# Kernel optimization log

Measured on AMD Instinct MI355X. Metric: run time of the kernel, lower is better.

## Reference

```python
import jax, jax.numpy as jnp
import numpy as np

B, NF, NB, E = 32768, 64, 33, 64  # batch, num_features, boundaries per feature, embedding size


def setup_inputs() -> dict:
    key = jax.random.key(0)
    kx, kb, kw = jax.random.split(key, 3)
    X = jax.random.normal(kx, (B, NF), dtype=jnp.float32)
    # strictly increasing per-feature boundaries: cumsum of positive steps
    steps = jax.random.uniform(kb, (NF, NB), dtype=jnp.float32, minval=0.05, maxval=0.2)
    bounds = jnp.cumsum(steps, axis=1) - 2.0  # roughly centered around the data range
    W = jax.random.normal(kw, (NF, NB - 1, E), dtype=jnp.float32) / np.sqrt(NB - 1).astype(np.float32)
    b = jnp.zeros((NF, E), dtype=jnp.float32)
    return {"X": X, "bounds": bounds, "W": W, "b": b}


def reference(X, bounds, W, b):
    # Piecewise-linear bin encoding, vectorized over all features at once.
    lo = bounds[:, :-1]            # [NF, NB-1]
    hi = bounds[:, 1:]             # [NF, NB-1]
    scale = hi - lo                # [NF, NB-1]
    x = X[:, :, None]              # [B, NF, 1]
    enc = (jax.nn.relu(x - lo[None]) - jax.nn.relu(x - hi[None])) / scale  # [B, NF, NB-1]
    # Per-feature Linear + ReLU (block-diagonal / grouped GEMM), then concat over features
    out = jax.nn.relu(jnp.einsum('bfi,fie->bfe', enc, W) + b[None])       # [B, NF, E]
    return out.reshape(X.shape[0], -1)                                     # [B, NF*E]
```

## Files before the change

### kernel.cpp

```cpp
#include <hip/hip_runtime.h>

#define B_TOT 32768
#define NF    64
#define NB    33
#define NSEG  32
#define E     64
#define BPB   256

__global__ __launch_bounds__(256) void pwl_kernel(
    const float* __restrict__ X,
    const float* __restrict__ bounds,
    const float* __restrict__ W,
    const float* __restrict__ bias,
    float* __restrict__ out)
{
    __shared__ __align__(16) float sW[NSEG][E];
    __shared__ __align__(16) float sP[NB][E];
    __shared__ float sBounds[NB];
    __shared__ float sFrac[BPB];
    __shared__ int   sJ[BPB];

    const int f   = blockIdx.x;
    const int tid = threadIdx.x;
    const int b0  = blockIdx.y * BPB;

    {
        const float4* Wg  = reinterpret_cast<const float4*>(W + f * (NSEG * E));
        float4*       sW4 = reinterpret_cast<float4*>(&sW[0][0]);
        sW4[tid]       = Wg[tid];
        sW4[tid + 256] = Wg[tid + 256];
        if (tid < NB) sBounds[tid] = bounds[f * NB + tid];
    }
    __syncthreads();

    if (tid < E) {
        float acc = bias[f * E + tid];
        sP[0][tid] = acc;
        #pragma unroll
        for (int i = 0; i < NSEG; ++i) {
            acc += sW[i][tid];
            sP[i + 1][tid] = acc;
        }
    }
    __syncthreads();

    {
        const float x = X[(b0 + tid) * NF + f];
        int c = 0;
        #pragma unroll
        for (int i = 0; i < NB; ++i) c += (sBounds[i] <= x) ? 1 : 0;
        int j = c - 1;
        j = (j < 0) ? 0 : ((j > NSEG - 1) ? NSEG - 1 : j);
        const float lo = sBounds[j];
        const float hi = sBounds[j + 1];
        float fr = (x - lo) / (hi - lo);
        fr = fminf(fmaxf(fr, 0.0f), 1.0f);
        sJ[tid]   = j;
        sFrac[tid] = fr;
    }
    __syncthreads();

    const int q = tid & 15;
    const int g = tid >> 4;
    const float4* sP4 = reinterpret_cast<const float4*>(&sP[0][0]);
    const float4* sW4 = reinterpret_cast<const float4*>(&sW[0][0]);
    float4* out4 = reinterpret_cast<float4*>(out);
    const int colbase = f * (E / 4) + q;

    #pragma unroll 4
    for (int k = 0; k < 16; ++k) {
        const int idx = k * 16 + g;
        const int   j  = sJ[idx];
        const float fr = sFrac[idx];
        const float4 p = sP4[j * 16 + q];
        const float4 w = sW4[j * 16 + q];
        float4 r;
        r.x = fmaxf(fmaf(fr, w.x, p.x), 0.0f);
        r.y = fmaxf(fmaf(fr, w.y, p.y), 0.0f);
        r.z = fmaxf(fmaf(fr, w.z, p.z), 0.0f);
        r.w = fmaxf(fmaf(fr, w.w, p.w), 0.0f);
        out4[(b0 + idx) * (NF * E / 4) + colbase] = r;
    }
}

extern "C" void kernel_launch(void* const* d_in, const int* in_sizes, int n_in,
                              void* d_out, int out_size, void* d_ws, size_t ws_size,
                              hipStream_t stream) {
    const float* X      = (const float*)d_in[0];
    const float* bounds = (const float*)d_in[1];
    const float* W      = (const float*)d_in[2];
    const float* bias   = (const float*)d_in[3];
    float* out          = (float*)d_out;

    dim3 grid(NF, B_TOT / BPB);
    dim3 block(256);
    pwl_kernel<<<grid, block, 0, stream>>>(X, bounds, W, bias, out);
}
```

Measured before the change: 537.9 us.

## Precompute prefix tables in separate kernel and tile by batch rows across all features

Moves the per-feature prefix-sum table into a small separate kernel that writes to workspace, so it is computed once instead of per block. The main kernel now tiles by 32 batch rows covering all 64 features, so each wave writes fully contiguous output rows instead of strided 256-byte chunks, and X is loaded coalesced. P and W rows are gathered from global memory, relying on L2/L1 caching (the tables total about 1 MB), in exchange for dropping the per-block shared-memory table builds. It adds a second launch and a workspace dependency.

```diff
diff --git a/kernel.cpp b/kernel.cpp
--- a/kernel.cpp
+++ b/kernel.cpp
@@ -5,81 +5,104 @@
 #define NB    33
 #define NSEG  32
 #define E     64
-#define BPB   256
+#define ROWS  32
+#define NBLK  (B_TOT / ROWS)
+#define BPAD  35
 
-__global__ __launch_bounds__(256) void pwl_kernel(
+__global__ __launch_bounds__(64) void prefix_kernel(
+    const float* __restrict__ W, const float* __restrict__ bias,
+    float* __restrict__ P)
+{
+    const int f = blockIdx.x;
+    const int e = threadIdx.x;
+    const float* Wf = W + f * (NSEG * E) + e;
+    float*       Pf = P + f * (NSEG * E) + e;
+    float acc = bias[f * E + e];
+    Pf[0] = acc;
+    #pragma unroll
+    for (int i = 0; i < NSEG - 1; ++i) {
+        acc += Wf[i * E];
+        Pf[(i + 1) * E] = acc;
+    }
+}
+
+__global__ __launch_bounds__(256, 4) void pwl_kernel(
     const float* __restrict__ X,
     const float* __restrict__ bounds,
     const float* __restrict__ W,
-    const float* __restrict__ bias,
+    const float* __restrict__ P,
     float* __restrict__ out)
 {
-    __shared__ __align__(16) float sW[NSEG][E];
-    __shared__ __align__(16) float sP[NB][E];
-    __shared__ float sBounds[NB];
-    __shared__ float sFrac[BPB];
-    __shared__ int   sJ[BPB];
-
-    const int f   = blockIdx.x;
+    __shared__ __align__(16) float  sX[ROWS][NF];
+    __shared__ float                sB[NF][BPAD];
+    __shared__ __align__(8)  float2 sJF[ROWS][NF];
     const int tid = threadIdx.x;
-    const int b0  = blockIdx.y * BPB;
+    const int b0  = blockIdx.x * ROWS;
 
     {
-        const float4* Wg  = reinterpret_cast<const float4*>(W + f * (NSEG * E));
-        float4*       sW4 = reinterpret_cast<float4*>(&sW[0][0]);
-        sW4[tid]       = Wg[tid];
-        sW4[tid + 256] = Wg[tid + 256];
-        if (tid < NB) sBounds[tid] = bounds[f * NB + tid];
+        const float4* Xg  = reinterpret_cast<const float4*>(X + b0 * NF);
+        float4*       sX4 = reinterpret_cast<float4*>(&sX[0][0]);
+        sX4[tid]       = Xg[tid];
+        sX4[tid + 256] = Xg[tid + 256];
+    }
+    for (int i = tid; i < NF * NB; i += 256) {
+        const int f = i / NB, k = i - f * NB;
+        sB[f][k] = bounds[i];
     }
     __syncthreads();
 
-    if (tid < E) {
-        float acc = bias[f * E + tid];
-        sP[0][tid] = acc;
+    {
+        const int f  = tid & 63;
+        const int rg = tid >> 6;
+        float bnd[NB];
         #pragma unroll
-        for (int i = 0; i < NSEG; ++i) {
-            acc += sW[i][tid];
-            sP[i + 1][tid] = acc;
+        for (int i = 0; i < NB; ++i) bnd[i] = sB[f][i];
+        #pragma unroll
+        for (int rr = 0; rr < ROWS / 4; ++rr) {
+            const int r = rg * (ROWS / 4) + rr;
+            const float x = sX[r][f];
+            int c = 0;
+            #pragma unroll
+            for (int i = 0; i < NB; ++i) c += (bnd[i] <= x) ? 1 : 0;
+            int j = c - 1;
+            j = (j < 0) ? 0 : ((j > NSEG - 1) ? NSEG - 1 : j);
+            const float lo = sB[f][j];
+            const float hi = sB[f][j + 1];
+            float fr = (x - lo) / (hi - lo);
+            fr = fminf(fmaxf(fr, 0.0f), 1.0f);
+            sJF[r][f] = make_float2(fr, __int_as_float(j));
         }
     }
     __syncthreads();
 
-    {
-        const float x = X[(b0 + tid) * NF + f];
-        int c = 0;
-        #pragma unroll
-        for (int i = 0; i < NB; ++i) c += (sBounds[i] <= x) ? 1 : 0;
-        int j = c - 1;
-        j = (j < 0) ? 0 : ((j > NSEG - 1) ? NSEG - 1 : j);
-        const float lo = sBounds[j];
-        const float hi = sBounds[j + 1];
-        float fr = (x - lo) / (hi - lo);
-        fr = fminf(fmaxf(fr, 0.0f), 1.0f);
-        sJ[tid]   = j;
-        sFrac[tid] = fr;
-    }
-    __syncthreads();
+    const int wave = tid >> 6;
+    const int lane = tid & 63;
+    const int q    = lane & 15;
+    const int fo   = lane >> 4;
+    const float4* P4   = reinterpret_cast<const float4*>(P);
+    const float4* W4   = reinterpret_cast<const float4*>(W);
+    float4*       out4 = reinterpret_cast<float4*>(out);
 
-    const int q = tid & 15;
-    const int g = tid >> 4;
-    const float4* sP4 = reinterpret_cast<const float4*>(&sP[0][0]);
-    const float4* sW4 = reinterpret_cast<const float4*>(&sW[0][0]);
-    float4* out4 = reinterpret_cast<float4*>(out);
-    const int colbase = f * (E / 4) + q;
-
-    #pragma unroll 4
-    for (int k = 0; k < 16; ++k) {
-        const int idx = k * 16 + g;
-        const int   j  = sJ[idx];
-        const float fr = sFrac[idx];
-        const float4 p = sP4[j * 16 + q];
-        const float4 w = sW4[j * 16 + q];
-        float4 r;
-        r.x = fmaxf(fmaf(fr, w.x, p.x), 0.0f);
-        r.y = fmaxf(fmaf(fr, w.y, p.y), 0.0f);
-        r.z = fmaxf(fmaf(fr, w.z, p.z), 0.0f);
-        r.w = fmaxf(fmaf(fr, w.w, p.w), 0.0f);
-        out4[(b0 + idx) * (NF * E / 4) + colbase] = r;
+    #pragma unroll
+    for (int rr = 0; rr < ROWS / 4; ++rr) {
+        const int r = wave * (ROWS / 4) + rr;
+        const long rowbase = (long)(b0 + r) * (NF * E / 4);
+        #pragma unroll 4
+        for (int fb = 0; fb < 16; ++fb) {
+            const int f = fb * 4 + fo;
+            const float2 jf = sJF[r][f];
+            const float fr  = jf.x;
+            const int   j   = __float_as_int(jf.y);
+            const int   off = (f * NSEG + j) * 16 + q;
+            const float4 p = P4[off];
+            const float4 w = W4[off];
+            float4 res;
+            res.x = fmaxf(fmaf(fr, w.x, p.x), 0.0f);
+            res.y = fmaxf(fmaf(fr, w.y, p.y), 0.0f);
+            res.z = fmaxf(fmaf(fr, w.z, p.z), 0.0f);
+            res.w = fmaxf(fmaf(fr, w.w, p.w), 0.0f);
+            out4[rowbase + fb * 64 + lane] = res;
+        }
     }
 }
 
@@ -90,9 +113,9 @@
     const float* bounds = (const float*)d_in[1];
     const float* W      = (const float*)d_in[2];
     const float* bias   = (const float*)d_in[3];
-    float* out          = (float*)d_out;
+    float* P   = (float*)d_ws;
+    float* out = (float*)d_out;
 
-    dim3 grid(NF, B_TOT / BPB);
-    dim3 block(256);
-    pwl_kernel<<<grid, block, 0, stream>>>(X, bounds, W, bias, out);
+    prefix_kernel<<<dim3(NF), dim3(E), 0, stream>>>(W, bias, P);
+    pwl_kernel<<<dim3(NBLK), dim3(256), 0, stream>>>(X, bounds, W, P, out);
 }
```

After: 542.4 us. No clear change (+0.8%).
